# Kernel tuning notes

Hardware: AMD Instinct MI355X
Metric: run time of the kernel (lower is better)

The kernel has to match this reference:

```python
import jax, jax.numpy as jnp
import numpy as np

B = 8          # number of point clouds
P = 2048       # points per cloud (equal-length segments)
D_FEAT = 16    # matched feature dim
BIG = 1e10     # mask value for cross-batch pairs

LOSS_WEIGHT = 1.0
COORD_WEIGHT = 1.0
FEAT_WEIGHT = 0.1


def setup_inputs() -> dict:
    key = jax.random.key(0)
    k1, k2, k3, k4 = jax.random.split(key, 4)
    n = B * P
    pred_coord = jax.random.normal(k1, (n, 3), dtype=jnp.float32) * 10.0
    target_coord = jax.random.normal(k2, (n, 3), dtype=jnp.float32) * 10.0
    pred_feat = jax.random.normal(k3, (n, D_FEAT), dtype=jnp.float32)
    target_feat = jax.random.normal(k4, (n, D_FEAT), dtype=jnp.float32)
    offsets = (jnp.arange(1, B + 1) * P).astype(jnp.int32)  # cumulative ends
    return {
        'pred_coord': pred_coord,
        'target_coord': target_coord,
        'pred_feat': pred_feat,
        'target_feat': target_feat,
        'pred_offset': offsets,
        'target_offset': offsets,
    }


def _batch_ids(offsets, n):
    # point i belongs to batch b where offsets[b-1] <= i < offsets[b]
    return jnp.searchsorted(offsets, jnp.arange(n), side='right')


def _lengths(offsets):
    prev = jnp.concatenate([jnp.zeros((1,), offsets.dtype), offsets[:-1]])
    return offsets - prev


def _nn_dist(x, y, xb, yb):
    # masked all-pairs squared distances [n, m]; per-batch KNN(k=1)
    d2 = (jnp.sum(x * x, axis=1)[:, None]
          - 2.0 * (x @ y.T)
          + jnp.sum(y * y, axis=1)[None, :])
    d2 = jnp.where(xb[:, None] == yb[None, :], d2, BIG)
    idx = jnp.argmin(d2, axis=1)
    nearest = y[idx]                          # gather nearest neighbor
    dist = jnp.sum((x - nearest) ** 2, axis=1)  # norm=2, recomputed as in torch
    return dist, idx


def _chamfer_dir(x, y, x_off, y_off):
    xb = _batch_ids(x_off, x.shape[0])
    yb = _batch_ids(y_off, y.shape[0])
    dist, idx = _nn_dist(x, y, xb, yb)
    seg = jax.ops.segment_sum(dist, xb, num_segments=B)
    lens = jnp.maximum(_lengths(x_off), 1).astype(dist.dtype)
    return seg / lens, idx                    # point_reduction='mean'


def reference(pred_coord, target_coord, pred_feat, target_feat,
              pred_offset, target_offset):
    cham_x, x_idx = _chamfer_dir(pred_coord, target_coord, pred_offset, target_offset)
    cham_y, _ = _chamfer_dir(target_coord, pred_coord, target_offset, pred_offset)
    # bidirectional sum, batch_reduction='mean' (weights None -> divide by B)
    coord_loss = jnp.sum(cham_x + cham_y) / B
    # matched feature MSE via pred->target nearest-neighbor indices
    nearest_feat = target_feat[x_idx]
    feat_loss = jnp.mean((pred_feat - nearest_feat) ** 2)
    loss = LOSS_WEIGHT * (COORD_WEIGHT * coord_loss + FEAT_WEIGHT * feat_loss)
    return (loss, coord_loss, feat_loss)
```

## Files before the change

kernel.cpp:

```cpp
#include <hip/hip_runtime.h>

#define BATCHES 8
#define PTS     2048
#define DFEAT   16
#define QPB     256
#define CCH     8
#define CPC     128
#define NQ      16384
#define NKEY    (2 * NQ)

__global__ __launch_bounds__(512) void
nn_kernel(const float* __restrict__ pred_coord,
          const float* __restrict__ target_coord,
          unsigned long long* __restrict__ keys) {
    __shared__ float4 cand[1024];
    __shared__ unsigned long long pk[CCH][QPB];

    const int bid   = blockIdx.x;
    const int dir   = bid >> 7;
    const int rem   = bid & 127;
    const int batch = rem >> 4;
    const int qg    = (rem & 15) >> 1;
    const int half  = rem & 1;
    const int tid   = threadIdx.x;
    const int lane  = tid & 63;
    const int chunk = tid >> 6;

    const float* x = (dir == 0) ? pred_coord   : target_coord;
    const float* y = (dir == 0) ? target_coord : pred_coord;

    const float* ybase = y + ((size_t)batch * PTS + half * 1024) * 3;
    for (int k = tid; k < 1024; k += 512) {
        float cx = ybase[3 * k], cy = ybase[3 * k + 1], cz = ybase[3 * k + 2];
        cand[k] = make_float4(cx, cy, cz, 0.5f * (cx * cx + cy * cy + cz * cz));
    }
    __syncthreads();

    const int qbase = batch * PTS + qg * QPB;
    float nax[4], nay[4], naz[4], hx[4];
    #pragma unroll
    for (int k = 0; k < 4; ++k) {
        int q = qbase + lane + 64 * k;
        float ax = x[3 * q], ay = x[3 * q + 1], az = x[3 * q + 2];
        nax[k] = -ax; nay[k] = -ay; naz[k] = -az;
        hx[k]  = 0.5f * (ax * ax + ay * ay + az * az);
    }

    const int jbase = chunk * CPC;
    float best[4] = {1e30f, 1e30f, 1e30f, 1e30f};
    int   bj[4]   = {0, 0, 0, 0};
    #pragma unroll 8
    for (int i = 0; i < CPC; ++i) {
        int j = jbase + i;
        float4 c = cand[j];
        #pragma unroll
        for (int k = 0; k < 4; ++k) {
            float s = fmaf(nax[k], c.x,
                      fmaf(nay[k], c.y,
                      fmaf(naz[k], c.z, hx[k] + c.w)));
            if (s < best[k]) { best[k] = s; bj[k] = j; }
        }
    }
    const unsigned int goff = half * 1024;
    #pragma unroll
    for (int k = 0; k < 4; ++k) {
        pk[chunk][lane + 64 * k] =
            ((unsigned long long)__float_as_uint(fmaxf(best[k], 0.f)) << 32)
            | (goff + (unsigned int)bj[k]);
    }
    __syncthreads();

    if (tid < QPB) {
        unsigned long long m = pk[0][tid];
        #pragma unroll
        for (int c = 1; c < CCH; ++c) {
            unsigned long long v = pk[c][tid];
            m = (v < m) ? v : m;
        }
        int q = qbase + tid;
        keys[(size_t)half * NKEY + (size_t)dir * NQ + q] = m;
    }
}

__global__ __launch_bounds__(256) void
merge_kernel(const float* __restrict__ pred_coord,
             const float* __restrict__ target_coord,
             const float* __restrict__ pred_feat,
             const float* __restrict__ target_feat,
             const unsigned long long* __restrict__ keys,
             float2* __restrict__ partials) {
    __shared__ float wa[4], wb[4];
    const int t   = blockIdx.x * 256 + threadIdx.x;
    const int dir = t >> 14;
    const int q   = t & (NQ - 1);
    const int batch = q >> 11;

    unsigned long long k0 = keys[t];
    unsigned long long k1 = keys[NKEY + t];
    unsigned long long m  = (k1 < k0) ? k1 : k0;
    const int j   = (int)(m & 0xffffffffu);
    const int row = batch * PTS + j;

    const float* x = (dir == 0) ? pred_coord   : target_coord;
    const float* y = (dir == 0) ? target_coord : pred_coord;
    float dx = x[3 * q]     - y[3 * row];
    float dy = x[3 * q + 1] - y[3 * row + 1];
    float dz = x[3 * q + 2] - y[3 * row + 2];
    float ds = dx * dx + dy * dy + dz * dz;

    float fs = 0.f;
    if (dir == 0) {
        const float4* pf = (const float4*)(pred_feat + (size_t)q * DFEAT);
        const float4* tf = (const float4*)(target_feat + (size_t)row * DFEAT);
        #pragma unroll
        for (int k = 0; k < 4; ++k) {
            float4 a = pf[k], b = tf[k];
            float d0 = a.x - b.x, d1 = a.y - b.y, d2 = a.z - b.z, d3 = a.w - b.w;
            fs += d0 * d0 + d1 * d1 + d2 * d2 + d3 * d3;
        }
    }

    #pragma unroll
    for (int off = 32; off > 0; off >>= 1) {
        ds += __shfl_down(ds, off);
        fs += __shfl_down(fs, off);
    }
    const int wave = threadIdx.x >> 6, lane = threadIdx.x & 63;
    if (lane == 0) { wa[wave] = ds; wb[wave] = fs; }
    __syncthreads();
    if (threadIdx.x == 0) {
        partials[blockIdx.x] = make_float2(wa[0] + wa[1] + wa[2] + wa[3],
                                           wb[0] + wb[1] + wb[2] + wb[3]);
    }
}

__global__ __launch_bounds__(128) void
final_kernel(const float2* __restrict__ partials, float* __restrict__ out) {
    __shared__ float a[2], b[2];
    const int tid = threadIdx.x;
    float2 p = partials[tid];
    float ds = p.x, fs = p.y;
    #pragma unroll
    for (int off = 32; off > 0; off >>= 1) {
        ds += __shfl_down(ds, off);
        fs += __shfl_down(fs, off);
    }
    const int wave = tid >> 6, lane = tid & 63;
    if (lane == 0) { a[wave] = ds; b[wave] = fs; }
    __syncthreads();
    if (tid == 0) {
        float dsum = a[0] + a[1];
        float fsum = b[0] + b[1];
        float coord_loss = dsum / (float)(BATCHES * PTS);
        float feat_loss  = fsum / (float)(NQ * DFEAT);
        float loss = coord_loss + 0.1f * feat_loss;
        out[0] = loss;
        out[1] = coord_loss;
        out[2] = feat_loss;
    }
}

extern "C" void kernel_launch(void* const* d_in, const int* in_sizes, int n_in,
                              void* d_out, int out_size, void* d_ws, size_t ws_size,
                              hipStream_t stream) {
    const float* pred_coord   = (const float*)d_in[0];
    const float* target_coord = (const float*)d_in[1];
    const float* pred_feat    = (const float*)d_in[2];
    const float* target_feat  = (const float*)d_in[3];

    unsigned long long* keys = (unsigned long long*)d_ws;
    float2* partials = (float2*)((char*)d_ws + 2ull * NKEY * sizeof(unsigned long long));

    nn_kernel<<<256, 512, 0, stream>>>(pred_coord, target_coord, keys);
    merge_kernel<<<128, 256, 0, stream>>>(pred_coord, target_coord,
                                          pred_feat, target_feat, keys, partials);
    final_kernel<<<1, 128, 0, stream>>>(partials, (float*)d_out);
}
```

Measured before the change: 81.89 us.

## Fuse final reduction into merge via atomics and reuse stored NN distance

Removes the separate final_kernel launch by having merge blocks atomically accumulate their partial sums and letting the last block, chosen by a ticket counter, write the outputs. The accumulators are zeroed inside nn_kernel. The merge step also stops re-gathering coordinates and instead uses twice the half-distance stored in the key, which skips the coordinate loads. In exchange, the distance now comes from the expanded-form computation rather than a direct recompute, so cancellation can change precision, and float atomics make the summation order nondeterministic.

```diff
diff --git a/kernel.cpp b/kernel.cpp
--- a/kernel.cpp
+++ b/kernel.cpp
@@ -8,11 +8,15 @@
 #define CPC     128
 #define NQ      16384
 #define NKEY    (2 * NQ)
+#define MERGE_BLOCKS 128
+
+struct WsTail { float acc_d; float acc_f; unsigned counter; };
 
 __global__ __launch_bounds__(512) void
 nn_kernel(const float* __restrict__ pred_coord,
           const float* __restrict__ target_coord,
-          unsigned long long* __restrict__ keys) {
+          unsigned long long* __restrict__ keys,
+          WsTail* __restrict__ tail) {
     __shared__ float4 cand[1024];
     __shared__ unsigned long long pk[CCH][QPB];
 
@@ -25,6 +29,10 @@
     const int tid   = threadIdx.x;
     const int lane  = tid & 63;
     const int chunk = tid >> 6;
+
+    if (bid == 0 && tid == 0) {
+        tail->acc_d = 0.f; tail->acc_f = 0.f; tail->counter = 0u;
+    }
 
     const float* x = (dir == 0) ? pred_coord   : target_coord;
     const float* y = (dir == 0) ? target_coord : pred_coord;
@@ -83,12 +91,11 @@
 }
 
 __global__ __launch_bounds__(256) void
-merge_kernel(const float* __restrict__ pred_coord,
-             const float* __restrict__ target_coord,
-             const float* __restrict__ pred_feat,
-             const float* __restrict__ target_feat,
-             const unsigned long long* __restrict__ keys,
-             float2* __restrict__ partials) {
+merge_final(const float* __restrict__ pred_feat,
+            const float* __restrict__ target_feat,
+            const unsigned long long* __restrict__ keys,
+            WsTail* __restrict__ tail,
+            float* __restrict__ out) {
     __shared__ float wa[4], wb[4];
     const int t   = blockIdx.x * 256 + threadIdx.x;
     const int dir = t >> 14;
@@ -98,18 +105,11 @@
     unsigned long long k0 = keys[t];
     unsigned long long k1 = keys[NKEY + t];
     unsigned long long m  = (k1 < k0) ? k1 : k0;
-    const int j   = (int)(m & 0xffffffffu);
-    const int row = batch * PTS + j;
 
-    const float* x = (dir == 0) ? pred_coord   : target_coord;
-    const float* y = (dir == 0) ? target_coord : pred_coord;
-    float dx = x[3 * q]     - y[3 * row];
-    float dy = x[3 * q + 1] - y[3 * row + 1];
-    float dz = x[3 * q + 2] - y[3 * row + 2];
-    float ds = dx * dx + dy * dy + dz * dz;
-
+    float ds = 2.0f * __uint_as_float((unsigned int)(m >> 32));
     float fs = 0.f;
     if (dir == 0) {
+        const int row = batch * PTS + (int)(m & 0xffffffffu);
         const float4* pf = (const float4*)(pred_feat + (size_t)q * DFEAT);
         const float4* tf = (const float4*)(target_feat + (size_t)row * DFEAT);
         #pragma unroll
@@ -128,35 +128,24 @@
     const int wave = threadIdx.x >> 6, lane = threadIdx.x & 63;
     if (lane == 0) { wa[wave] = ds; wb[wave] = fs; }
     __syncthreads();
+
     if (threadIdx.x == 0) {
-        partials[blockIdx.x] = make_float2(wa[0] + wa[1] + wa[2] + wa[3],
-                                           wb[0] + wb[1] + wb[2] + wb[3]);
-    }
-}
-
-__global__ __launch_bounds__(128) void
-final_kernel(const float2* __restrict__ partials, float* __restrict__ out) {
-    __shared__ float a[2], b[2];
-    const int tid = threadIdx.x;
-    float2 p = partials[tid];
-    float ds = p.x, fs = p.y;
-    #pragma unroll
-    for (int off = 32; off > 0; off >>= 1) {
-        ds += __shfl_down(ds, off);
-        fs += __shfl_down(fs, off);
-    }
-    const int wave = tid >> 6, lane = tid & 63;
-    if (lane == 0) { a[wave] = ds; b[wave] = fs; }
-    __syncthreads();
-    if (tid == 0) {
-        float dsum = a[0] + a[1];
-        float fsum = b[0] + b[1];
-        float coord_loss = dsum / (float)(BATCHES * PTS);
-        float feat_loss  = fsum / (float)(NQ * DFEAT);
-        float loss = coord_loss + 0.1f * feat_loss;
-        out[0] = loss;
-        out[1] = coord_loss;
-        out[2] = feat_loss;
+        float bds = wa[0] + wa[1] + wa[2] + wa[3];
+        float bfs = wb[0] + wb[1] + wb[2] + wb[3];
+        atomicAdd(&tail->acc_d, bds);
+        atomicAdd(&tail->acc_f, bfs);
+        __threadfence();
+        unsigned ticket = atomicAdd(&tail->counter, 1u);
+        if (ticket == MERGE_BLOCKS - 1) {
+            __threadfence();
+            float dsum = atomicAdd(&tail->acc_d, 0.f);
+            float fsum = atomicAdd(&tail->acc_f, 0.f);
+            float coord_loss = dsum / (float)(BATCHES * PTS);
+            float feat_loss  = fsum / (float)(NQ * DFEAT);
+            out[0] = coord_loss + 0.1f * feat_loss;
+            out[1] = coord_loss;
+            out[2] = feat_loss;
+        }
     }
 }
 
@@ -169,10 +158,9 @@
     const float* target_feat  = (const float*)d_in[3];
 
     unsigned long long* keys = (unsigned long long*)d_ws;
-    float2* partials = (float2*)((char*)d_ws + 2ull * NKEY * sizeof(unsigned long long));
+    WsTail* tail = (WsTail*)((char*)d_ws + 2ull * NKEY * sizeof(unsigned long long));
 
-    nn_kernel<<<256, 512, 0, stream>>>(pred_coord, target_coord, keys);
-    merge_kernel<<<128, 256, 0, stream>>>(pred_coord, target_coord,
-                                          pred_feat, target_feat, keys, partials);
-    final_kernel<<<1, 128, 0, stream>>>(partials, (float*)d_out);
+    nn_kernel<<<256, 512, 0, stream>>>(pred_coord, target_coord, keys, tail);
+    merge_final<<<MERGE_BLOCKS, 256, 0, stream>>>(pred_feat, target_feat,
+                                                  keys, tail, (float*)d_out);
 }
```

After: 84.26 us. 1.03x slower.

## Split candidates into quarters, skip argmin for reverse direction, reuse key distances

Applied to the files above, without the earlier changes.

Candidate sets are split four ways instead of two, doubling the grid to 512 blocks so more CUs are busy. The per-query half-norm is added once after the inner loop rather than on every candidate. The reverse direction only needs the minimum distance, so it uses fminf with no index tracking. The merge kernel takes the distance directly from the packed key (times two) instead of gathering coordinates and recomputing it. This drops the exact recomputation the reference does, so small float errors from the expanded-form distance now reach the loss.

```diff
diff --git a/kernel.cpp b/kernel.cpp
--- a/kernel.cpp
+++ b/kernel.cpp
@@ -3,40 +3,38 @@
 #define BATCHES 8
 #define PTS     2048
 #define DFEAT   16
-#define QPB     256
-#define CCH     8
-#define CPC     128
 #define NQ      16384
 #define NKEY    (2 * NQ)
 
-__global__ __launch_bounds__(512) void
+__global__ __launch_bounds__(512, 4) void
 nn_kernel(const float* __restrict__ pred_coord,
           const float* __restrict__ target_coord,
           unsigned long long* __restrict__ keys) {
-    __shared__ float4 cand[1024];
-    __shared__ unsigned long long pk[CCH][QPB];
+    __shared__ float4 cand[512];
+    __shared__ unsigned long long pk[8][256];
 
-    const int bid   = blockIdx.x;
-    const int dir   = bid >> 7;
-    const int rem   = bid & 127;
-    const int batch = rem >> 4;
-    const int qg    = (rem & 15) >> 1;
-    const int half  = rem & 1;
-    const int tid   = threadIdx.x;
-    const int lane  = tid & 63;
-    const int chunk = tid >> 6;
+    const int bid     = blockIdx.x;
+    const int dir     = bid >> 8;
+    const int rem     = bid & 255;
+    const int batch   = rem >> 5;
+    const int qg      = (rem >> 2) & 7;
+    const int quarter = rem & 3;
+    const int tid     = threadIdx.x;
+    const int lane    = tid & 63;
+    const int wv      = tid >> 6;
 
     const float* x = (dir == 0) ? pred_coord   : target_coord;
     const float* y = (dir == 0) ? target_coord : pred_coord;
 
-    const float* ybase = y + ((size_t)batch * PTS + half * 1024) * 3;
-    for (int k = tid; k < 1024; k += 512) {
+    const float* ybase = y + ((size_t)batch * PTS + quarter * 512) * 3;
+    {
+        int k = tid;
         float cx = ybase[3 * k], cy = ybase[3 * k + 1], cz = ybase[3 * k + 2];
         cand[k] = make_float4(cx, cy, cz, 0.5f * (cx * cx + cy * cy + cz * cz));
     }
     __syncthreads();
 
-    const int qbase = batch * PTS + qg * QPB;
+    const int qbase = batch * PTS + qg * 256;
     float nax[4], nay[4], naz[4], hx[4];
     #pragma unroll
     for (int k = 0; k < 4; ++k) {
@@ -46,46 +44,57 @@
         hx[k]  = 0.5f * (ax * ax + ay * ay + az * az);
     }
 
-    const int jbase = chunk * CPC;
+    const int jbase = wv * 64;
     float best[4] = {1e30f, 1e30f, 1e30f, 1e30f};
     int   bj[4]   = {0, 0, 0, 0};
-    #pragma unroll 8
-    for (int i = 0; i < CPC; ++i) {
-        int j = jbase + i;
-        float4 c = cand[j];
-        #pragma unroll
-        for (int k = 0; k < 4; ++k) {
-            float s = fmaf(nax[k], c.x,
-                      fmaf(nay[k], c.y,
-                      fmaf(naz[k], c.z, hx[k] + c.w)));
-            if (s < best[k]) { best[k] = s; bj[k] = j; }
+    if (dir == 0) {
+        #pragma unroll 8
+        for (int i = 0; i < 64; ++i) {
+            int j = jbase + i;
+            float4 c = cand[j];
+            #pragma unroll
+            for (int k = 0; k < 4; ++k) {
+                float s = fmaf(nax[k], c.x,
+                          fmaf(nay[k], c.y,
+                          fmaf(naz[k], c.z, c.w)));
+                if (s < best[k]) { best[k] = s; bj[k] = j; }
+            }
+        }
+    } else {
+        #pragma unroll 8
+        for (int i = 0; i < 64; ++i) {
+            float4 c = cand[jbase + i];
+            #pragma unroll
+            for (int k = 0; k < 4; ++k) {
+                float s = fmaf(nax[k], c.x,
+                          fmaf(nay[k], c.y,
+                          fmaf(naz[k], c.z, c.w)));
+                best[k] = fminf(best[k], s);
+            }
         }
     }
-    const unsigned int goff = half * 1024;
+    const unsigned int goff = quarter * 512;
     #pragma unroll
     for (int k = 0; k < 4; ++k) {
-        pk[chunk][lane + 64 * k] =
-            ((unsigned long long)__float_as_uint(fmaxf(best[k], 0.f)) << 32)
+        pk[wv][lane + 64 * k] =
+            ((unsigned long long)__float_as_uint(fmaxf(best[k] + hx[k], 0.f)) << 32)
             | (goff + (unsigned int)bj[k]);
     }
     __syncthreads();
 
-    if (tid < QPB) {
+    if (tid < 256) {
         unsigned long long m = pk[0][tid];
         #pragma unroll
-        for (int c = 1; c < CCH; ++c) {
+        for (int c = 1; c < 8; ++c) {
             unsigned long long v = pk[c][tid];
             m = (v < m) ? v : m;
         }
-        int q = qbase + tid;
-        keys[(size_t)half * NKEY + (size_t)dir * NQ + q] = m;
+        keys[(size_t)quarter * NKEY + (size_t)dir * NQ + qbase + tid] = m;
     }
 }
 
 __global__ __launch_bounds__(256) void
-merge_kernel(const float* __restrict__ pred_coord,
-             const float* __restrict__ target_coord,
-             const float* __restrict__ pred_feat,
+merge_kernel(const float* __restrict__ pred_feat,
              const float* __restrict__ target_feat,
              const unsigned long long* __restrict__ keys,
              float2* __restrict__ partials) {
@@ -95,21 +104,17 @@
     const int q   = t & (NQ - 1);
     const int batch = q >> 11;
 
-    unsigned long long k0 = keys[t];
-    unsigned long long k1 = keys[NKEY + t];
-    unsigned long long m  = (k1 < k0) ? k1 : k0;
-    const int j   = (int)(m & 0xffffffffu);
-    const int row = batch * PTS + j;
+    unsigned long long m = keys[t];
+    #pragma unroll
+    for (int qq = 1; qq < 4; ++qq) {
+        unsigned long long v = keys[(size_t)qq * NKEY + t];
+        m = (v < m) ? v : m;
+    }
 
-    const float* x = (dir == 0) ? pred_coord   : target_coord;
-    const float* y = (dir == 0) ? target_coord : pred_coord;
-    float dx = x[3 * q]     - y[3 * row];
-    float dy = x[3 * q + 1] - y[3 * row + 1];
-    float dz = x[3 * q + 2] - y[3 * row + 2];
-    float ds = dx * dx + dy * dy + dz * dz;
-
+    float ds = 2.0f * __uint_as_float((unsigned int)(m >> 32));
     float fs = 0.f;
     if (dir == 0) {
+        const int row = batch * PTS + (int)(m & 0xffffffffu);
         const float4* pf = (const float4*)(pred_feat + (size_t)q * DFEAT);
         const float4* tf = (const float4*)(target_feat + (size_t)row * DFEAT);
         #pragma unroll
@@ -153,8 +158,7 @@
         float fsum = b[0] + b[1];
         float coord_loss = dsum / (float)(BATCHES * PTS);
         float feat_loss  = fsum / (float)(NQ * DFEAT);
-        float loss = coord_loss + 0.1f * feat_loss;
-        out[0] = loss;
+        out[0] = coord_loss + 0.1f * feat_loss;
         out[1] = coord_loss;
         out[2] = feat_loss;
     }
@@ -169,10 +173,9 @@
     const float* target_feat  = (const float*)d_in[3];
 
     unsigned long long* keys = (unsigned long long*)d_ws;
-    float2* partials = (float2*)((char*)d_ws + 2ull * NKEY * sizeof(unsigned long long));
+    float2* partials = (float2*)((char*)d_ws + 4ull * NKEY * sizeof(unsigned long long));
 
-    nn_kernel<<<256, 512, 0, stream>>>(pred_coord, target_coord, keys);
-    merge_kernel<<<128, 256, 0, stream>>>(pred_coord, target_coord,
-                                          pred_feat, target_feat, keys, partials);
+    nn_kernel<<<512, 512, 0, stream>>>(pred_coord, target_coord, keys);
+    merge_kernel<<<128, 256, 0, stream>>>(pred_feat, target_feat, keys, partials);
     final_kernel<<<1, 128, 0, stream>>>(partials, (float*)d_out);
 }
```

New measurement: 76.64 us. -6.4%, faster.
